# Kernel tuning notes

Hardware: AMD Instinct MI355X
Metric: run time of the kernel (lower is better)

The kernel has to match this reference:

```python
import jax, jax.numpy as jnp
import numpy as np

B, P, NB = 16, 10000, 10


def setup_inputs() -> dict:
    key = jax.random.key(0)
    k1, k2, k3, k4 = jax.random.split(key, 4)
    geofeature = jax.random.normal(k1, (B, P, 9), dtype=jnp.float32)
    # neighbor indices into padded T; 0 is the zero-padding row
    nb = jax.random.randint(k2, (P, NB), 0, P + 1)
    reconmatrix = jax.random.normal(k3, (P, P), dtype=jnp.float32) / np.float32(np.sqrt(P))
    vdiff = jax.random.normal(k4, (P, NB, 3), dtype=jnp.float32)
    return {"geofeature": geofeature, "nb": nb, "reconmatrix": reconmatrix, "vdiff": vdiff}


def _ftoT(f):
    # f: [B, P, 9]. First 3 = log-rotation, last 6 = symmetric scale/shear.
    logr = f[..., :3]
    x, y, z = logr[..., 0], logr[..., 1], logr[..., 2]
    theta = jnp.sqrt(jnp.sum(logr * logr, axis=-1))  # [B, P]
    zero = jnp.zeros_like(x)
    # matches torch gather [6,0,1,3,6,2,4,5,6] over [x,y,z,-x,-y,-z,0]:
    # [[0, x, y], [-x, 0, z], [-y, -z, 0]]
    K = jnp.stack([zero, x, y, -x, zero, z, -y, -z, zero], axis=-1)
    K = K.reshape(f.shape[0], f.shape[1], 3, 3)
    cond = theta == 0
    safe_theta = jnp.where(cond, jnp.ones_like(theta), theta)
    Kn = K / safe_theta[..., None, None]
    st = jnp.sin(safe_theta)[..., None, None]
    ct = jnp.cos(safe_theta)[..., None, None]
    I = jnp.eye(3, dtype=f.dtype)
    R_rod = I + Kn * st + jnp.matmul(Kn, Kn) * (1.0 - ct)
    R = jnp.where(cond[..., None, None], I, R_rod)
    # S symmetric from features 3..8 via gather pattern [3,4,5,4,6,7,5,7,8]
    s3, s4, s5, s6, s7, s8 = (f[..., i] for i in range(3, 9))
    S = jnp.stack([s3, s4, s5, s4, s6, s7, s5, s7, s8], axis=-1)
    S = S.reshape(f.shape[0], f.shape[1], 3, 3)
    return jnp.matmul(R, S)  # [B, P, 3, 3]


def reference(geofeature, nb, reconmatrix, vdiff):
    T = _ftoT(geofeature)  # [B, P, 3, 3]
    padded = jnp.concatenate([jnp.zeros((T.shape[0], 1, 3, 3), T.dtype), T], axis=1)
    nb_T = padded[:, nb]                    # [B, P, NB, 3, 3] neighbor gather
    sum_T = nb_T + T[:, :, None]            # [B, P, NB, 3, 3]
    bdiff = jnp.einsum('bpnde,pne->bpnd', sum_T, vdiff)  # [B, P, NB, 3]
    bvec = jnp.sum(bdiff, axis=2)           # [B, P, 3]
    v = jnp.einsum('vp,bpe->bve', reconmatrix, bvec)     # [B, P, 3]
    return v
```

## Files before the change

kernel.cpp:

```cpp
#include <hip/hip_runtime.h>
#include <math.h>

#define B_    16
#define P_    10000
#define NB_   10
#define KBTOT 313
#define KBPAD 328
#define NSMAX 8

typedef __attribute__((ext_vector_type(8))) short bf16x8;
typedef __attribute__((ext_vector_type(4))) float f32x4;

static __device__ __forceinline__ unsigned short f2bf(float f) {
    unsigned u = __float_as_uint(f);
    u += 0x7fffu + ((u >> 16) & 1u);
    return (unsigned short)(u >> 16);
}

__global__ __launch_bounds__(256) void ftoT_kernel(const float* __restrict__ f,
                                                   float* __restrict__ Tm2) {
    int t = blockIdx.x * blockDim.x + threadIdx.x;
    if (t >= B_ * P_) return;
    int p = t >> 4, b = t & 15;
    const float* fp = f + ((size_t)b * P_ + p) * 9;
    float x = fp[0], y = fp[1], z = fp[2];
    float s3 = fp[3], s4 = fp[4], s5 = fp[5], s6 = fp[6], s7 = fp[7], s8 = fp[8];
    float th2 = x * x + y * y + z * z;
    float R00, R01, R02, R10, R11, R12, R20, R21, R22;
    if (th2 == 0.0f) {
        R00 = 1; R01 = 0; R02 = 0; R10 = 0; R11 = 1; R12 = 0; R20 = 0; R21 = 0; R22 = 1;
    } else {
        float theta = sqrtf(th2);
        float inv = 1.0f / theta;
        float kx = x * inv, ky = y * inv, kz = z * inv;
        float st = sinf(theta);
        float omc = 1.0f - cosf(theta);
        R00 = 1.0f - omc * (kx * kx + ky * ky);
        R01 = kx * st - omc * (ky * kz);
        R02 = ky * st + omc * (kx * kz);
        R10 = -kx * st - omc * (ky * kz);
        R11 = 1.0f - omc * (kx * kx + kz * kz);
        R12 = kz * st - omc * (kx * ky);
        R20 = -ky * st + omc * (kx * kz);
        R21 = -kz * st - omc * (kx * ky);
        R22 = 1.0f - omc * (ky * ky + kz * kz);
    }
    float* o = Tm2 + (size_t)t * 12;
    o[0] = R00 * s3 + R01 * s4 + R02 * s5;
    o[1] = R00 * s4 + R01 * s6 + R02 * s7;
    o[2] = R00 * s5 + R01 * s7 + R02 * s8;
    o[3] = R10 * s3 + R11 * s4 + R12 * s5;
    o[4] = R10 * s4 + R11 * s6 + R12 * s7;
    o[5] = R10 * s5 + R11 * s7 + R12 * s8;
    o[6] = R20 * s3 + R21 * s4 + R22 * s5;
    o[7] = R20 * s4 + R21 * s6 + R22 * s7;
    o[8] = R20 * s5 + R21 * s7 + R22 * s8;
    o[9] = 0.0f; o[10] = 0.0f; o[11] = 0.0f;
}

__global__ __launch_bounds__(256) void bvec_kernel(const float* __restrict__ Tm2,
                                                   const int* __restrict__ nb,
                                                   const float* __restrict__ vdiff,
                                                   unsigned short* __restrict__ Bf) {
    int tid = threadIdx.x;
    int bl = tid & 15, pl = tid >> 4;
    int p = blockIdx.x * 16 + pl;
    if (p >= P_) return;

    const float4* Tow = (const float4*)(Tm2 + ((size_t)p * 16 + bl) * 12);
    float4 o0 = Tow[0], o1 = Tow[1], o2 = Tow[2];

    float a0 = 0, a1 = 0, a2 = 0, vs0 = 0, vs1 = 0, vs2 = 0;
#pragma unroll
    for (int n = 0; n < NB_; n++) {
        int idx = nb[p * NB_ + n];
        const float* vd = vdiff + ((size_t)p * NB_ + n) * 3;
        float v0 = vd[0], v1 = vd[1], v2 = vd[2];
        vs0 += v0; vs1 += v1; vs2 += v2;
        if (idx > 0) {
            const float4* Tp = (const float4*)(Tm2 + ((size_t)(idx - 1) * 16 + bl) * 12);
            float4 q0 = Tp[0], q1 = Tp[1], q2 = Tp[2];
            a0 += q0.x * v0 + q0.y * v1 + q0.z * v2;
            a1 += q0.w * v0 + q1.x * v1 + q1.y * v2;
            a2 += q1.z * v0 + q1.w * v1 + q2.x * v2;
        }
    }
    a0 += o0.x * vs0 + o0.y * vs1 + o0.z * vs2;
    a1 += o0.w * vs0 + o1.x * vs1 + o1.y * vs2;
    a2 += o1.z * vs0 + o1.w * vs1 + o2.x * vs2;

    int kb = p >> 5, ii = p & 7, quad = (p >> 3) & 3;
    float vals[3] = {a0, a1, a2};
#pragma unroll
    for (int d = 0; d < 3; d++) {
        int j = bl * 3 + d;
        int t = j >> 4;
        int ln = quad * 16 + (j & 15);
        Bf[(((size_t)kb * 3 + t) * 64 + ln) * 8 + ii] = f2bf(vals[d]);
    }
}

__global__ __launch_bounds__(256) void gemm_mfma(const float* __restrict__ recon,
                                                 const unsigned short* __restrict__ Bf,
                                                 float* __restrict__ part, int KBC) {
    int l = threadIdx.x & 63;
    int w = threadIdx.x >> 6;
    int r0 = (blockIdx.x * 4 + w) * 16;
    if (r0 >= P_) return;
    int y = blockIdx.y;
    int kb0 = y * KBC;
    int n = l & 15, quad = l >> 4;
    int r = r0 + n;
    const float* ap = recon + (size_t)r * P_;
    const bf16x8* Bv = (const bf16x8*)Bf;

    f32x4 acc0 = {0, 0, 0, 0}, acc1 = {0, 0, 0, 0}, acc2 = {0, 0, 0, 0};

#pragma unroll 2
    for (int kb = kb0; kb < kb0 + KBC; ++kb) {
        int k = kb * 32 + quad * 8;
        bf16x8 a;
        if (k < P_) {
            const float4* apk = (const float4*)(ap + k);
            float4 x0 = apk[0], x1 = apk[1];
            a[0] = (short)f2bf(x0.x); a[1] = (short)f2bf(x0.y);
            a[2] = (short)f2bf(x0.z); a[3] = (short)f2bf(x0.w);
            a[4] = (short)f2bf(x1.x); a[5] = (short)f2bf(x1.y);
            a[6] = (short)f2bf(x1.z); a[7] = (short)f2bf(x1.w);
        } else {
            a = (bf16x8)0;
        }
        bf16x8 b0 = Bv[((size_t)kb * 3 + 0) * 64 + l];
        bf16x8 b1 = Bv[((size_t)kb * 3 + 1) * 64 + l];
        bf16x8 b2 = Bv[((size_t)kb * 3 + 2) * 64 + l];
        acc0 = __builtin_amdgcn_mfma_f32_16x16x32_bf16(a, b0, acc0, 0, 0, 0);
        acc1 = __builtin_amdgcn_mfma_f32_16x16x32_bf16(a, b1, acc1, 0, 0, 0);
        acc2 = __builtin_amdgcn_mfma_f32_16x16x32_bf16(a, b2, acc2, 0, 0, 0);
    }

    float* base = part + (size_t)y * (48 * P_);
    int rs = r0 + quad * 4;
    f32x4 accs[3] = {acc0, acc1, acc2};
#pragma unroll
    for (int t = 0; t < 3; t++) {
        int j = t * 16 + n;
        float4 st = make_float4(accs[t][0], accs[t][1], accs[t][2], accs[t][3]);
        *(float4*)(base + (size_t)j * P_ + rs) = st;
    }
}

__global__ __launch_bounds__(256) void reduce_kernel(const float* __restrict__ part,
                                                     float* __restrict__ out, int NS) {
    int i = blockIdx.x * blockDim.x + threadIdx.x;
    if (i >= 48 * P_) return;
    float s = 0.0f;
    for (int z = 0; z < NS; z++) s += part[(size_t)z * (48 * P_) + i];
    int j = i / P_;
    int r = i - j * P_;
    int b = j / 3;
    int d = j - 3 * b;
    out[((size_t)b * P_ + r) * 3 + d] = s;
}

extern "C" void kernel_launch(void* const* d_in, const int* in_sizes, int n_in,
                              void* d_out, int out_size, void* d_ws, size_t ws_size,
                              hipStream_t stream) {
    const float* geo   = (const float*)d_in[0];
    const int*   nb    = (const int*)d_in[1];
    const float* recon = (const float*)d_in[2];
    const float* vdiff = (const float*)d_in[3];
    float* out = (float*)d_out;

    const size_t Tm2F = (size_t)B_ * P_ * 12;
    const size_t BfU  = (size_t)KBPAD * 3 * 64 * 8;
    const size_t BfF  = (BfU + 1) / 2;
    float*          Tm2  = (float*)d_ws;
    unsigned short* Bf   = (unsigned short*)(Tm2 + Tm2F);
    float*          part = Tm2 + Tm2F + BfF;

    size_t ws_floats = ws_size / 4;
    size_t used = Tm2F + BfF;
    size_t avail = (ws_floats > used) ? (ws_floats - used) : 0;
    int NS = (int)(avail / ((size_t)48 * P_));
    if (NS > NSMAX) NS = NSMAX;
    if (NS < 1) NS = 1;
    int KBC = (320 + NS - 1) / NS;

    hipMemsetAsync(Bf, 0, BfU * sizeof(unsigned short), stream);
    int BP = B_ * P_;
    hipLaunchKernelGGL(ftoT_kernel, dim3((BP + 255) / 256), dim3(256), 0, stream, geo, Tm2);
    hipLaunchKernelGGL(bvec_kernel, dim3((P_ + 15) / 16), dim3(256), 0, stream,
                       Tm2, nb, vdiff, Bf);
    hipLaunchKernelGGL(gemm_mfma, dim3((P_ + 63) / 64, NS), dim3(256), 0, stream,
                       recon, Bf, part, KBC);
    hipLaunchKernelGGL(reduce_kernel, dim3((48 * P_ + 255) / 256), dim3(256), 0, stream,
                       part, out, NS);
}
```

Before: 567.0 us.

## Register-tile GEMM to 32 rows per wave with prefetch; stage B-tiles in LDS

Result: no change. 571.6 us (+0.8%).

```diff
diff --git a/kernel.cpp b/kernel.cpp
--- a/kernel.cpp
+++ b/kernel.cpp
@@ -5,8 +5,7 @@
 #define P_    10000
 #define NB_   10
 #define KBTOT 313
-#define KBPAD 328
-#define NSMAX 8
+#define NSMAX 16
 
 typedef __attribute__((ext_vector_type(8))) short bf16x8;
 typedef __attribute__((ext_vector_type(4))) float f32x4;
@@ -58,94 +57,148 @@
     o[9] = 0.0f; o[10] = 0.0f; o[11] = 0.0f;
 }
 
-__global__ __launch_bounds__(256) void bvec_kernel(const float* __restrict__ Tm2,
+__global__ __launch_bounds__(512) void bvec_kernel(const float* __restrict__ Tm2,
                                                    const int* __restrict__ nb,
                                                    const float* __restrict__ vdiff,
                                                    unsigned short* __restrict__ Bf) {
+    __shared__ int   s_nb[320];
+    __shared__ float s_vd[960];
+    __shared__ unsigned short s_B[3 * 64 * 8];
     int tid = threadIdx.x;
-    int bl = tid & 15, pl = tid >> 4;
-    int p = blockIdx.x * 16 + pl;
-    if (p >= P_) return;
-
-    const float4* Tow = (const float4*)(Tm2 + ((size_t)p * 16 + bl) * 12);
-    float4 o0 = Tow[0], o1 = Tow[1], o2 = Tow[2];
-
-    float a0 = 0, a1 = 0, a2 = 0, vs0 = 0, vs1 = 0, vs2 = 0;
-#pragma unroll
-    for (int n = 0; n < NB_; n++) {
-        int idx = nb[p * NB_ + n];
-        const float* vd = vdiff + ((size_t)p * NB_ + n) * 3;
-        float v0 = vd[0], v1 = vd[1], v2 = vd[2];
-        vs0 += v0; vs1 += v1; vs2 += v2;
-        if (idx > 0) {
-            const float4* Tp = (const float4*)(Tm2 + ((size_t)(idx - 1) * 16 + bl) * 12);
-            float4 q0 = Tp[0], q1 = Tp[1], q2 = Tp[2];
-            a0 += q0.x * v0 + q0.y * v1 + q0.z * v2;
-            a1 += q0.w * v0 + q1.x * v1 + q1.y * v2;
-            a2 += q1.z * v0 + q1.w * v1 + q2.x * v2;
-        }
-    }
-    a0 += o0.x * vs0 + o0.y * vs1 + o0.z * vs2;
-    a1 += o0.w * vs0 + o1.x * vs1 + o1.y * vs2;
-    a2 += o1.z * vs0 + o1.w * vs1 + o2.x * vs2;
-
-    int kb = p >> 5, ii = p & 7, quad = (p >> 3) & 3;
-    float vals[3] = {a0, a1, a2};
-#pragma unroll
-    for (int d = 0; d < 3; d++) {
-        int j = bl * 3 + d;
-        int t = j >> 4;
-        int ln = quad * 16 + (j & 15);
-        Bf[(((size_t)kb * 3 + t) * 64 + ln) * 8 + ii] = f2bf(vals[d]);
-    }
-}
-
-__global__ __launch_bounds__(256) void gemm_mfma(const float* __restrict__ recon,
-                                                 const unsigned short* __restrict__ Bf,
-                                                 float* __restrict__ part, int KBC) {
+    int kb = blockIdx.x;
+    int p0 = kb * 32;
+    for (int i = tid; i < 320; i += 512) {
+        int g = p0 * 10 + i;
+        s_nb[i] = (g < P_ * NB_) ? nb[g] : 0;
+    }
+    for (int i = tid; i < 960; i += 512) {
+        int g = p0 * 30 + i;
+        s_vd[i] = (g < P_ * NB_ * 3) ? vdiff[g] : 0.0f;
+    }
+    for (int i = tid; i < 768; i += 512) ((unsigned*)s_B)[i] = 0u;
+    __syncthreads();
+
+    int pl = tid >> 4, bl = tid & 15;
+    int p = p0 + pl;
+    if (p < P_) {
+        const float4* Tow = (const float4*)(Tm2 + ((size_t)p * 16 + bl) * 12);
+        float4 o0 = Tow[0], o1 = Tow[1], o2v = Tow[2];
+        float a0 = 0, a1 = 0, a2 = 0, vs0 = 0, vs1 = 0, vs2 = 0;
+#pragma unroll
+        for (int nn = 0; nn < NB_; nn++) {
+            int idx = s_nb[pl * 10 + nn];
+            float v0 = s_vd[pl * 30 + nn * 3 + 0];
+            float v1 = s_vd[pl * 30 + nn * 3 + 1];
+            float v2 = s_vd[pl * 30 + nn * 3 + 2];
+            vs0 += v0; vs1 += v1; vs2 += v2;
+            if (idx > 0) {
+                const float4* Tp = (const float4*)(Tm2 + ((size_t)(idx - 1) * 16 + bl) * 12);
+                float4 q0 = Tp[0], q1 = Tp[1], q2 = Tp[2];
+                a0 += q0.x * v0 + q0.y * v1 + q0.z * v2;
+                a1 += q0.w * v0 + q1.x * v1 + q1.y * v2;
+                a2 += q1.z * v0 + q1.w * v1 + q2.x * v2;
+            }
+        }
+        a0 += o0.x * vs0 + o0.y * vs1 + o0.z * vs2;
+        a1 += o0.w * vs0 + o1.x * vs1 + o1.y * vs2;
+        a2 += o1.z * vs0 + o1.w * vs1 + o2v.x * vs2;
+
+        int ii = pl & 7, quad = pl >> 3;
+        float vals[3] = {a0, a1, a2};
+#pragma unroll
+        for (int d = 0; d < 3; d++) {
+            int j = bl * 3 + d;
+            int t = j >> 4;
+            int ln = quad * 16 + (j & 15);
+            s_B[((size_t)t * 64 + ln) * 8 + ii] = f2bf(vals[d]);
+        }
+    }
+    __syncthreads();
+    const uint4* src = (const uint4*)s_B;
+    uint4* dst = (uint4*)(Bf + (size_t)kb * (3 * 64 * 8));
+    if (tid < 192) dst[tid] = src[tid];
+}
+
+struct Pref {
+    float4 x00, x01, x10, x11;
+    bf16x8 b0, b1, b2;
+};
+
+__global__ __launch_bounds__(256, 4) void gemm_mfma(const float* __restrict__ recon,
+                                                    const unsigned short* __restrict__ Bf,
+                                                    float* __restrict__ part, int KBC) {
     int l = threadIdx.x & 63;
     int w = threadIdx.x >> 6;
-    int r0 = (blockIdx.x * 4 + w) * 16;
-    if (r0 >= P_) return;
+    int r0 = blockIdx.x * 128 + w * 32;
     int y = blockIdx.y;
     int kb0 = y * KBC;
+    int kbend = kb0 + KBC;
+    if (kbend > KBTOT) kbend = KBTOT;
     int n = l & 15, quad = l >> 4;
-    int r = r0 + n;
-    const float* ap = recon + (size_t)r * P_;
+    int rA = r0 + n;       if (rA >= P_) rA = P_ - 1;
+    int rB = r0 + 16 + n;  if (rB >= P_) rB = P_ - 1;
+    const float* ap0 = recon + (size_t)rA * P_;
+    const float* ap1 = recon + (size_t)rB * P_;
     const bf16x8* Bv = (const bf16x8*)Bf;
 
-    f32x4 acc0 = {0, 0, 0, 0}, acc1 = {0, 0, 0, 0}, acc2 = {0, 0, 0, 0};
-
-#pragma unroll 2
-    for (int kb = kb0; kb < kb0 + KBC; ++kb) {
+    f32x4 acc[6];
+#pragma unroll
+    for (int i = 0; i < 6; i++) acc[i] = (f32x4){0, 0, 0, 0};
+
+    auto loadP = [&](int kb, Pref& Pr) {
         int k = kb * 32 + quad * 8;
+        if (k + 8 <= P_) {
+            Pr.x00 = *(const float4*)(ap0 + k);
+            Pr.x01 = *(const float4*)(ap0 + k + 4);
+            Pr.x10 = *(const float4*)(ap1 + k);
+            Pr.x11 = *(const float4*)(ap1 + k + 4);
+        } else {
+            Pr.x00 = Pr.x01 = Pr.x10 = Pr.x11 = make_float4(0, 0, 0, 0);
+        }
+        size_t o = (size_t)kb * 192 + l;
+        Pr.b0 = Bv[o];
+        Pr.b1 = Bv[o + 64];
+        Pr.b2 = Bv[o + 128];
+    };
+    auto cvt = [&](float4 lo, float4 hi) -> bf16x8 {
         bf16x8 a;
-        if (k < P_) {
-            const float4* apk = (const float4*)(ap + k);
-            float4 x0 = apk[0], x1 = apk[1];
-            a[0] = (short)f2bf(x0.x); a[1] = (short)f2bf(x0.y);
-            a[2] = (short)f2bf(x0.z); a[3] = (short)f2bf(x0.w);
-            a[4] = (short)f2bf(x1.x); a[5] = (short)f2bf(x1.y);
-            a[6] = (short)f2bf(x1.z); a[7] = (short)f2bf(x1.w);
-        } else {
-            a = (bf16x8)0;
-        }
-        bf16x8 b0 = Bv[((size_t)kb * 3 + 0) * 64 + l];
-        bf16x8 b1 = Bv[((size_t)kb * 3 + 1) * 64 + l];
-        bf16x8 b2 = Bv[((size_t)kb * 3 + 2) * 64 + l];
-        acc0 = __builtin_amdgcn_mfma_f32_16x16x32_bf16(a, b0, acc0, 0, 0, 0);
-        acc1 = __builtin_amdgcn_mfma_f32_16x16x32_bf16(a, b1, acc1, 0, 0, 0);
-        acc2 = __builtin_amdgcn_mfma_f32_16x16x32_bf16(a, b2, acc2, 0, 0, 0);
+        a[0] = (short)f2bf(lo.x); a[1] = (short)f2bf(lo.y);
+        a[2] = (short)f2bf(lo.z); a[3] = (short)f2bf(lo.w);
+        a[4] = (short)f2bf(hi.x); a[5] = (short)f2bf(hi.y);
+        a[6] = (short)f2bf(hi.z); a[7] = (short)f2bf(hi.w);
+        return a;
+    };
+
+    Pref cur, nxt;
+    loadP(kb0, cur);
+    for (int kb = kb0; kb < kbend; ++kb) {
+        int kbn = (kb + 1 < kbend) ? kb + 1 : kb;
+        loadP(kbn, nxt);
+        bf16x8 A0 = cvt(cur.x00, cur.x01);
+        bf16x8 A1 = cvt(cur.x10, cur.x11);
+        acc[0] = __builtin_amdgcn_mfma_f32_16x16x32_bf16(A0, cur.b0, acc[0], 0, 0, 0);
+        acc[1] = __builtin_amdgcn_mfma_f32_16x16x32_bf16(A0, cur.b1, acc[1], 0, 0, 0);
+        acc[2] = __builtin_amdgcn_mfma_f32_16x16x32_bf16(A0, cur.b2, acc[2], 0, 0, 0);
+        acc[3] = __builtin_amdgcn_mfma_f32_16x16x32_bf16(A1, cur.b0, acc[3], 0, 0, 0);
+        acc[4] = __builtin_amdgcn_mfma_f32_16x16x32_bf16(A1, cur.b1, acc[4], 0, 0, 0);
+        acc[5] = __builtin_amdgcn_mfma_f32_16x16x32_bf16(A1, cur.b2, acc[5], 0, 0, 0);
+        cur = nxt;
     }
 
     float* base = part + (size_t)y * (48 * P_);
-    int rs = r0 + quad * 4;
-    f32x4 accs[3] = {acc0, acc1, acc2};
+    int rs0 = r0 + quad * 4;
+    int rs1 = r0 + 16 + quad * 4;
 #pragma unroll
     for (int t = 0; t < 3; t++) {
         int j = t * 16 + n;
-        float4 st = make_float4(accs[t][0], accs[t][1], accs[t][2], accs[t][3]);
-        *(float4*)(base + (size_t)j * P_ + rs) = st;
+        if (rs0 < P_) {
+            f32x4 a = acc[t];
+            *(float4*)(base + (size_t)j * P_ + rs0) = make_float4(a[0], a[1], a[2], a[3]);
+        }
+        if (rs1 < P_) {
+            f32x4 a = acc[3 + t];
+            *(float4*)(base + (size_t)j * P_ + rs1) = make_float4(a[0], a[1], a[2], a[3]);
+        }
     }
 }
 
@@ -172,7 +225,7 @@
     float* out = (float*)d_out;
 
     const size_t Tm2F = (size_t)B_ * P_ * 12;
-    const size_t BfU  = (size_t)KBPAD * 3 * 64 * 8;
+    const size_t BfU  = (size_t)KBTOT * 3 * 64 * 8;
     const size_t BfF  = (BfU + 1) / 2;
     float*          Tm2  = (float*)d_ws;
     unsigned short* Bf   = (unsigned short*)(Tm2 + Tm2F);
@@ -184,15 +237,15 @@
     int NS = (int)(avail / ((size_t)48 * P_));
     if (NS > NSMAX) NS = NSMAX;
     if (NS < 1) NS = 1;
-    int KBC = (320 + NS - 1) / NS;
-
-    hipMemsetAsync(Bf, 0, BfU * sizeof(unsigned short), stream);
+    int KBC = (KBTOT + NS - 1) / NS;
+    int NSeff = (KBTOT + KBC - 1) / KBC;
+
     int BP = B_ * P_;
     hipLaunchKernelGGL(ftoT_kernel, dim3((BP + 255) / 256), dim3(256), 0, stream, geo, Tm2);
-    hipLaunchKernelGGL(bvec_kernel, dim3((P_ + 15) / 16), dim3(256), 0, stream,
+    hipLaunchKernelGGL(bvec_kernel, dim3(KBTOT), dim3(512), 0, stream,
                        Tm2, nb, vdiff, Bf);
-    hipLaunchKernelGGL(gemm_mfma, dim3((P_ + 63) / 64, NS), dim3(256), 0, stream,
+    hipLaunchKernelGGL(gemm_mfma, dim3((P_ + 127) / 128, NSeff), dim3(256), 0, stream,
                        recon, Bf, part, KBC);
     hipLaunchKernelGGL(reduce_kernel, dim3((48 * P_ + 255) / 256), dim3(256), 0, stream,
-                       part, out, NS);
-}
+                       part, out, NSeff);
+}
```
